# Performance work log

Hardware: AMD Instinct MI355X
Metric: run time of the kernel (lower is better)

The kernel has to match this reference:

```python
import jax, jax.numpy as jnp
import numpy as np

B, H, S, D = 4, 16, 1024, 64
TEMPERATURE = 8.0  # sqrt(D)


def setup_inputs() -> dict:
    key = jax.random.key(0)
    k1, k2, k3, k4, k5, k6 = jax.random.split(key, 6)
    return {
        "q": jax.random.normal(k1, (B, H, S, D), dtype=jnp.float32),
        "k": jax.random.normal(k2, (B, H, S, D), dtype=jnp.float32),
        "v": jax.random.normal(k3, (B, H, S, D), dtype=jnp.float32),
        "mask": jax.random.randint(k4, (B, 1, 1, S), 0, 2, dtype=jnp.int32),
        "adj_matrix": jax.random.normal(k5, (B, S, S), dtype=jnp.float32),
        "dist_matrix": jax.random.uniform(k6, (B, S, S), dtype=jnp.float32),
    }


def reference(q, k, v, mask, adj_matrix, dist_matrix):
    # attn = (q / temperature) @ k^T  -> [B,H,S,S]
    attn = jnp.einsum("bhqd,bhkd->bhqk", q / TEMPERATURE, k)

    # distance-based rescaling: (1 + e) / (1 + exp(1 - dist)), broadcast over heads
    dist = dist_matrix[:, None, :, :]  # [B,1,S,S]
    one = jnp.float32(1.0)
    rescaled = (one + jnp.exp(one)) / (one + jnp.exp(one - dist))
    attn = jax.nn.relu(attn) * rescaled

    # additive adjacency bias, broadcast over heads
    attn = attn + adj_matrix[:, None, :, :]

    # mask fill
    attn = jnp.where(mask == 0, jnp.float32(-1e9), attn)

    attn = jax.nn.softmax(attn, axis=-1)  # dropout p used in eval -> identity
    output = jnp.einsum("bhqk,bhkd->bhqd", attn, v)
    return (output, attn)
```

## Files before the change

kernel.cpp:

```cpp
#include <hip/hip_runtime.h>
#include <hip/hip_bf16.h>

#define NB 4
#define NH 16
#define NS 1024
#define ND 64
#define NBH (NB * NH)
#define NELEM ((size_t)NBH * NS * ND)

typedef __bf16 bf16x8 __attribute__((ext_vector_type(8)));
typedef float f32x4 __attribute__((ext_vector_type(4)));
typedef unsigned short u16x8 __attribute__((ext_vector_type(8)));
typedef unsigned short u16x4 __attribute__((ext_vector_type(4)));


__global__ __launch_bounds__(256) void conv_hilo(const float* __restrict__ src,
                                                 unsigned short* __restrict__ hi,
                                                 unsigned short* __restrict__ lo,
                                                 float scale, int n4) {
    int i = blockIdx.x * 256 + threadIdx.x;
    if (i >= n4) return;
    f32x4 x = ((const f32x4*)src)[i];
    u16x4 h, l;
#pragma unroll
    for (int j = 0; j < 4; ++j) {
        float xs = x[j] * scale;
        __bf16 hb = (__bf16)xs;
        h[j] = __builtin_bit_cast(unsigned short, hb);
        l[j] = __builtin_bit_cast(unsigned short, (__bf16)(xs - (float)hb));
    }
    ((u16x4*)hi)[i] = h;
    ((u16x4*)lo)[i] = l;
}

__global__ __launch_bounds__(256) void conv_vt(const float* __restrict__ V,
                                               unsigned short* __restrict__ Vt) {
    int i = blockIdx.x * 256 + threadIdx.x;
    int bh = i >> 12;
    int kb = (i >> 6) & 63;
    int d  = i & 63;
    const float* vp = V + ((size_t)(bh * NS + kb * 16)) * ND + d;
    unsigned short* op = Vt + ((size_t)(bh * ND + d)) * NS + kb * 16;
    u16x8 o0, o1;
#pragma unroll
    for (int r = 0; r < 8; ++r) o0[r] = __builtin_bit_cast(unsigned short, (__bf16)vp[r * ND]);
#pragma unroll
    for (int r = 0; r < 8; ++r) o1[r] = __builtin_bit_cast(unsigned short, (__bf16)vp[(r + 8) * ND]);
    *(u16x8*)op = o0;
    *(u16x8*)(op + 8) = o1;
}

__global__ __launch_bounds__(256) void fused_attn_pre(
    const unsigned short* __restrict__ Qhi, const unsigned short* __restrict__ Qlo,
    const unsigned short* __restrict__ Khi, const unsigned short* __restrict__ Klo,
    const unsigned short* __restrict__ Vt,
    const int* __restrict__ mask, const float* __restrict__ adj, const float* __restrict__ dist,
    float* __restrict__ out_g, float* __restrict__ attn_g)
{
    const int tid  = (int)threadIdx.x;
    const int lane = tid & 63;
    const int wid  = tid >> 6;
    const int qi   = lane & 15;
    const int g    = lane >> 4;

    int bid = (int)blockIdx.x;
    bid = (bid & 7) * (NBH * 64 / 8) + (bid >> 3);
    const int qt = bid & 63;
    const int bh = bid >> 6;
    const int b  = bh >> 4;

    __shared__ __align__(16) unsigned char smem[4 * 16 * 256 * 2 + 512];
    unsigned short* Plds = (unsigned short*)smem;
    float* red_m = (float*)(smem + 32768);
    float* red_l = red_m + 64;
    typedef float outp_t[16][68];
    outp_t* outp = (outp_t*)smem;

    const int qglob = qt * 16 + qi;
    const int kw    = wid * 256;

    bf16x8 qh[2], ql[2];
    {
        const size_t qo = ((size_t)(bh * NS + qglob)) * ND + g * 8;
        qh[0] = __builtin_bit_cast(bf16x8, *(const u16x8*)(Qhi + qo));
        qh[1] = __builtin_bit_cast(bf16x8, *(const u16x8*)(Qhi + qo + 32));
        ql[0] = __builtin_bit_cast(bf16x8, *(const u16x8*)(Qlo + qo));
        ql[1] = __builtin_bit_cast(bf16x8, *(const u16x8*)(Qlo + qo + 32));
    }

    f32x4 acc[16];
    {
        const f32x4 z = {0.f, 0.f, 0.f, 0.f};
#pragma unroll
        for (int t = 0; t < 16; ++t) acc[t] = z;
    }
#pragma unroll
    for (int t = 0; t < 16; ++t) {
        const size_t ko = ((size_t)(bh * NS + kw + t * 16 + qi)) * ND + g * 8;
#pragma unroll
        for (int c = 0; c < 2; ++c) {
            bf16x8 kh = __builtin_bit_cast(bf16x8, *(const u16x8*)(Khi + ko + c * 32));
            bf16x8 kl = __builtin_bit_cast(bf16x8, *(const u16x8*)(Klo + ko + c * 32));
            acc[t] = __builtin_amdgcn_mfma_f32_16x16x32_bf16(kh, qh[c], acc[t], 0, 0, 0);
            acc[t] = __builtin_amdgcn_mfma_f32_16x16x32_bf16(kl, qh[c], acc[t], 0, 0, 0);
            acc[t] = __builtin_amdgcn_mfma_f32_16x16x32_bf16(kh, ql[c], acc[t], 0, 0, 0);
        }
    }

    const float* adjR  = adj  + ((size_t)(b * NS + qglob)) * NS;
    const float* distR = dist + ((size_t)(b * NS + qglob)) * NS;
    const int*   maskR = mask + b * NS;
    const float  CE = 3.7182817f;

#pragma unroll
    for (int t = 0; t < 16; ++t) {
        const int k0 = kw + t * 16 + g * 4;
        f32x4 a4 = *(const f32x4*)(adjR + k0);
        f32x4 d4 = *(const f32x4*)(distR + k0);
        int4  m4 = *(const int4*)(maskR + k0);
        int   mm[4] = {m4.x, m4.y, m4.z, m4.w};
#pragma unroll
        for (int r = 0; r < 4; ++r) {
            float s = fmaxf(acc[t][r], 0.f);
            float resc = CE * __builtin_amdgcn_rcpf(1.f + __expf(1.f - d4[r]));
            s = s * resc + a4[r];
            acc[t][r] = (mm[r] == 0) ? -1.0e9f : s;
        }
    }

    float m = -3.0e38f;
#pragma unroll
    for (int t = 0; t < 16; ++t)
#pragma unroll
        for (int r = 0; r < 4; ++r) m = fmaxf(m, acc[t][r]);
    m = fmaxf(m, __shfl_xor(m, 16, 64));
    m = fmaxf(m, __shfl_xor(m, 32, 64));
    if (g == 0) red_m[wid * 16 + qi] = m;
    __syncthreads();
    const float mf = fmaxf(fmaxf(red_m[qi], red_m[16 + qi]),
                           fmaxf(red_m[32 + qi], red_m[48 + qi]));

    float l = 0.f;
#pragma unroll
    for (int t = 0; t < 16; ++t)
#pragma unroll
        for (int r = 0; r < 4; ++r) {
            float e = __expf(acc[t][r] - mf);
            acc[t][r] = e;
            l += e;
        }
    l += __shfl_xor(l, 16, 64);
    l += __shfl_xor(l, 32, 64);
    if (g == 0) red_l[wid * 16 + qi] = l;
    __syncthreads();
    const float lf = red_l[qi] + red_l[16 + qi] + red_l[32 + qi] + red_l[48 + qi];
    const float inv = __builtin_amdgcn_rcpf(lf);

    float* attnR = attn_g + ((size_t)(bh * NS + qglob)) * NS;
    unsigned short* Pw = Plds + wid * (16 * 256);
#pragma unroll
    for (int t = 0; t < 16; ++t) {
        const int kloc = t * 16 + g * 4;
        f32x4 e4;
#pragma unroll
        for (int r = 0; r < 4; ++r) e4[r] = acc[t][r] * inv;
        __builtin_nontemporal_store(e4, (f32x4*)(attnR + kw + kloc));

        unsigned int p01 = ((unsigned int)__builtin_bit_cast(unsigned short, (__bf16)e4[0]))
                         | ((unsigned int)__builtin_bit_cast(unsigned short, (__bf16)e4[1]) << 16);
        unsigned int p23 = ((unsigned int)__builtin_bit_cast(unsigned short, (__bf16)e4[2]))
                         | ((unsigned int)__builtin_bit_cast(unsigned short, (__bf16)e4[3]) << 16);
        const int u = kloc >> 2;
        const int c = u >> 1;
        unsigned long long pk = (unsigned long long)p01 | ((unsigned long long)p23 << 32);
        *(unsigned long long*)((char*)Pw + qi * 512 + ((c ^ (qi & 7)) << 4) + (u & 1) * 8) = pk;
    }
    __syncthreads();

    f32x4 o[4];
    {
        const f32x4 z = {0.f, 0.f, 0.f, 0.f};
#pragma unroll
        for (int dt = 0; dt < 4; ++dt) o[dt] = z;
    }
    const unsigned short* vtb = Vt + ((size_t)bh * ND) * NS;
#pragma unroll
    for (int j = 0; j < 8; ++j) {
        const int c = j * 4 + g;
        const u16x8 praw = *(const u16x8*)((const char*)Pw + qi * 512 + ((c ^ (qi & 7)) << 4));
        const bf16x8 pa = __builtin_bit_cast(bf16x8, praw);
#pragma unroll
        for (int dt = 0; dt < 4; ++dt) {
            const bf16x8 vb = __builtin_bit_cast(bf16x8,
                *(const u16x8*)(vtb + (size_t)(dt * 16 + qi) * NS + kw + j * 32 + g * 8));
            o[dt] = __builtin_amdgcn_mfma_f32_16x16x32_bf16(pa, vb, o[dt], 0, 0, 0);
        }
    }
    __syncthreads();

#pragma unroll
    for (int dt = 0; dt < 4; ++dt)
#pragma unroll
        for (int r = 0; r < 4; ++r)
            outp[wid][g * 4 + r][dt * 16 + qi] = o[dt][r];
    __syncthreads();
    {
        const int qrow = tid >> 4;
        const int d0   = (tid & 15) * 4;
        f32x4 s = *(const f32x4*)(&outp[0][qrow][d0]);
#pragma unroll
        for (int w = 1; w < 4; ++w) s += *(const f32x4*)(&outp[w][qrow][d0]);
        __builtin_nontemporal_store(s, (f32x4*)(out_g + ((size_t)(bh * NS + qt * 16 + qrow)) * ND + d0));
    }
}

__global__ __launch_bounds__(256) void fused_attn_kernel(
    const float* __restrict__ Q, const float* __restrict__ K, const float* __restrict__ V,
    const int* __restrict__ mask, const float* __restrict__ adj, const float* __restrict__ dist,
    float* __restrict__ out_g, float* __restrict__ attn_g)
{
    const int tid  = (int)threadIdx.x;
    const int lane = tid & 63;
    const int wid  = tid >> 6;
    const int qi   = lane & 15;
    const int g    = lane >> 4;

    const int bid = (int)blockIdx.x;
    const int qt  = bid & 63;
    const int bh  = bid >> 6;
    const int b   = bh >> 4;

    __shared__ __align__(16) unsigned short Plds[4][16 * 256];
    __shared__ __align__(16) float outp[4][16][68];
    __shared__ float red_m[4][16];
    __shared__ float red_l[4][16];

    const int qglob = qt * 16 + qi;
    const int kw    = wid * 256;

    bf16x8 qh[2], ql[2];
    {
        const float* qp = Q + (bh * NS + qglob) * ND + g * 8;
#pragma unroll
        for (int c = 0; c < 2; ++c) {
            f32x4 f0 = *(const f32x4*)(qp + c * 32);
            f32x4 f1 = *(const f32x4*)(qp + c * 32 + 4);
#pragma unroll
            for (int j = 0; j < 4; ++j) {
                float xh = f0[j] * 0.125f;
                __bf16 hb = (__bf16)xh;
                qh[c][j] = hb; ql[c][j] = (__bf16)(xh - (float)hb);
                float xl = f1[j] * 0.125f;
                __bf16 hb2 = (__bf16)xl;
                qh[c][j + 4] = hb2; ql[c][j + 4] = (__bf16)(xl - (float)hb2);
            }
        }
    }

    f32x4 acc[16];
    {
        const f32x4 z = {0.f, 0.f, 0.f, 0.f};
#pragma unroll
        for (int t = 0; t < 16; ++t) acc[t] = z;
    }
#pragma unroll
    for (int t = 0; t < 16; ++t) {
        const float* kp = K + (bh * NS + kw + t * 16 + qi) * ND + g * 8;
#pragma unroll
        for (int c = 0; c < 2; ++c) {
            f32x4 f0 = *(const f32x4*)(kp + c * 32);
            f32x4 f1 = *(const f32x4*)(kp + c * 32 + 4);
            bf16x8 kh, kl;
#pragma unroll
            for (int j = 0; j < 4; ++j) {
                __bf16 hb = (__bf16)f0[j];
                kh[j] = hb; kl[j] = (__bf16)(f0[j] - (float)hb);
                __bf16 hb2 = (__bf16)f1[j];
                kh[j + 4] = hb2; kl[j + 4] = (__bf16)(f1[j] - (float)hb2);
            }
            acc[t] = __builtin_amdgcn_mfma_f32_16x16x32_bf16(kh, qh[c], acc[t], 0, 0, 0);
            acc[t] = __builtin_amdgcn_mfma_f32_16x16x32_bf16(kl, qh[c], acc[t], 0, 0, 0);
            acc[t] = __builtin_amdgcn_mfma_f32_16x16x32_bf16(kh, ql[c], acc[t], 0, 0, 0);
        }
    }

    const float* adjR  = adj  + (b * NS + qglob) * (size_t)NS;
    const float* distR = dist + (b * NS + qglob) * (size_t)NS;
    const int*   maskR = mask + b * NS;
    const float  CE = 3.7182817f;

#pragma unroll
    for (int t = 0; t < 16; ++t) {
        const int k0 = kw + t * 16 + g * 4;
        f32x4 a4 = *(const f32x4*)(adjR + k0);
        f32x4 d4 = *(const f32x4*)(distR + k0);
        int4  m4 = *(const int4*)(maskR + k0);
        int   mm[4] = {m4.x, m4.y, m4.z, m4.w};
#pragma unroll
        for (int r = 0; r < 4; ++r) {
            float s = fmaxf(acc[t][r], 0.f);
            float resc = CE * __builtin_amdgcn_rcpf(1.f + __expf(1.f - d4[r]));
            s = s * resc + a4[r];
            acc[t][r] = (mm[r] == 0) ? -1.0e9f : s;
        }
    }

    float m = -3.0e38f;
#pragma unroll
    for (int t = 0; t < 16; ++t)
#pragma unroll
        for (int r = 0; r < 4; ++r) m = fmaxf(m, acc[t][r]);
    m = fmaxf(m, __shfl_xor(m, 16, 64));
    m = fmaxf(m, __shfl_xor(m, 32, 64));
    if (g == 0) red_m[wid][qi] = m;
    __syncthreads();
    const float mf = fmaxf(fmaxf(red_m[0][qi], red_m[1][qi]),
                           fmaxf(red_m[2][qi], red_m[3][qi]));

    float l = 0.f;
#pragma unroll
    for (int t = 0; t < 16; ++t)
#pragma unroll
        for (int r = 0; r < 4; ++r) {
            float e = __expf(acc[t][r] - mf);
            acc[t][r] = e;
            l += e;
        }
    l += __shfl_xor(l, 16, 64);
    l += __shfl_xor(l, 32, 64);
    if (g == 0) red_l[wid][qi] = l;
    __syncthreads();
    const float lf = red_l[0][qi] + red_l[1][qi] + red_l[2][qi] + red_l[3][qi];
    const float inv = __builtin_amdgcn_rcpf(lf);

    float* attnR = attn_g + (bh * NS + qglob) * (size_t)NS;
    unsigned short* Pw = &Plds[wid][0];
#pragma unroll
    for (int t = 0; t < 16; ++t) {
        const int kloc = t * 16 + g * 4;
        f32x4 e4;
#pragma unroll
        for (int r = 0; r < 4; ++r) e4[r] = acc[t][r] * inv;
        __builtin_nontemporal_store(e4, (f32x4*)(attnR + kw + kloc));

        unsigned int p01 = ((unsigned int)__builtin_bit_cast(unsigned short, (__bf16)e4[0]))
                         | ((unsigned int)__builtin_bit_cast(unsigned short, (__bf16)e4[1]) << 16);
        unsigned int p23 = ((unsigned int)__builtin_bit_cast(unsigned short, (__bf16)e4[2]))
                         | ((unsigned int)__builtin_bit_cast(unsigned short, (__bf16)e4[3]) << 16);
        const int u = kloc >> 2;
        const int c = u >> 1;
        unsigned long long pk = (unsigned long long)p01 | ((unsigned long long)p23 << 32);
        *(unsigned long long*)((char*)Pw + qi * 512 + ((c ^ (qi & 7)) << 4) + (u & 1) * 8) = pk;
    }
    __syncthreads();

    f32x4 o[4];
    {
        const f32x4 z = {0.f, 0.f, 0.f, 0.f};
#pragma unroll
        for (int dt = 0; dt < 4; ++dt) o[dt] = z;
    }
    const float* vbase = V + (bh * NS + kw) * (size_t)ND;
#pragma unroll
    for (int j = 0; j < 8; ++j) {
        const int c = j * 4 + g;
        const u16x8 praw = *(const u16x8*)((const char*)Pw + qi * 512 + ((c ^ (qi & 7)) << 4));
        const bf16x8 pa = __builtin_bit_cast(bf16x8, praw);
        const float* vp0 = vbase + (j * 32 + g * 8) * ND + qi;
#pragma unroll
        for (int dt = 0; dt < 4; ++dt) {
            bf16x8 vb;
            const float* vp = vp0 + dt * 16;
#pragma unroll
            for (int r = 0; r < 8; ++r) vb[r] = (__bf16)vp[r * ND];
            o[dt] = __builtin_amdgcn_mfma_f32_16x16x32_bf16(pa, vb, o[dt], 0, 0, 0);
        }
    }

#pragma unroll
    for (int dt = 0; dt < 4; ++dt)
#pragma unroll
        for (int r = 0; r < 4; ++r)
            outp[wid][g * 4 + r][dt * 16 + qi] = o[dt][r];
    __syncthreads();
    {
        const int qrow = tid >> 4;
        const int d0   = (tid & 15) * 4;
        f32x4 s = *(const f32x4*)(&outp[0][qrow][d0]);
#pragma unroll
        for (int w = 1; w < 4; ++w) s += *(const f32x4*)(&outp[w][qrow][d0]);
        __builtin_nontemporal_store(s, (f32x4*)(out_g + (bh * NS + qt * 16 + qrow) * (size_t)ND + d0));
    }
}

extern "C" void kernel_launch(void* const* d_in, const int* in_sizes, int n_in,
                              void* d_out, int out_size, void* d_ws, size_t ws_size,
                              hipStream_t stream) {
    const float* Q    = (const float*)d_in[0];
    const float* K    = (const float*)d_in[1];
    const float* V    = (const float*)d_in[2];
    const int*   mask = (const int*)d_in[3];
    const float* adj  = (const float*)d_in[4];
    const float* dist = (const float*)d_in[5];
    float* out  = (float*)d_out;
    float* attn = out + NELEM;

    const size_t need = NELEM * 2 * 5;
    if (ws_size >= need) {
        unsigned short* Qhi = (unsigned short*)d_ws;
        unsigned short* Qlo = Qhi + NELEM;
        unsigned short* Khi = Qlo + NELEM;
        unsigned short* Klo = Khi + NELEM;
        unsigned short* Vt  = Klo + NELEM;
        const int n4 = (int)(NELEM / 4);
        conv_hilo<<<dim3(n4 / 256), 256, 0, stream>>>(Q, Qhi, Qlo, 0.125f, n4);
        conv_hilo<<<dim3(n4 / 256), 256, 0, stream>>>(K, Khi, Klo, 1.0f, n4);
        conv_vt<<<dim3(NBH * ND * (NS / 16) / 256), 256, 0, stream>>>(V, Vt);
        fused_attn_pre<<<dim3(NBH * 64), 256, 0, stream>>>(Qhi, Qlo, Khi, Klo, Vt,
                                                           mask, adj, dist, out, attn);
    } else {
        fused_attn_kernel<<<dim3(NBH * 64), 256, 0, stream>>>(Q, K, V, mask, adj, dist, out, attn);
    }
}
```

Measured before the change: 587.7 us.

## Stage attn writes through LDS for coalesced row stores and interleave QK with epilogue

The attention-probability output is now staged per wave in shared memory with an XOR swizzle, then written back so that each lane stores contiguous 16-byte chunks along a row instead of scattered per-lane row fragments. The QK MFMA chain is folded into the epilogue loop so the K, adj, dist and mask loads for a tile are issued together. Launch bounds now request two blocks per SM. The staging costs extra barriers and LDS traffic, and the occupancy hint may force register spills.

```diff
diff --git a/kernel.cpp b/kernel.cpp
--- a/kernel.cpp
+++ b/kernel.cpp
@@ -50,7 +50,7 @@
     *(u16x8*)(op + 8) = o1;
 }
 
-__global__ __launch_bounds__(256) void fused_attn_pre(
+__global__ __launch_bounds__(256, 2) void fused_attn_pre(
     const unsigned short* __restrict__ Qhi, const unsigned short* __restrict__ Qlo,
     const unsigned short* __restrict__ Khi, const unsigned short* __restrict__ Klo,
     const unsigned short* __restrict__ Vt,
@@ -62,6 +62,8 @@
     const int wid  = tid >> 6;
     const int qi   = lane & 15;
     const int g    = lane >> 4;
+    const int l31  = lane & 31;
+    const int rhalf = lane >> 5;
 
     int bid = (int)blockIdx.x;
     bid = (bid & 7) * (NBH * 64 / 8) + (bid >> 3);
@@ -69,7 +71,7 @@
     const int bh = bid >> 6;
     const int b  = bh >> 4;
 
-    __shared__ __align__(16) unsigned char smem[4 * 16 * 256 * 2 + 512];
+    __shared__ __align__(16) unsigned char smem[4 * 8192 + 512];
     unsigned short* Plds = (unsigned short*)smem;
     float* red_m = (float*)(smem + 32768);
     float* red_l = red_m + 64;
@@ -88,43 +90,40 @@
         ql[1] = __builtin_bit_cast(bf16x8, *(const u16x8*)(Qlo + qo + 32));
     }
 
-    f32x4 acc[16];
-    {
-        const f32x4 z = {0.f, 0.f, 0.f, 0.f};
-#pragma unroll
-        for (int t = 0; t < 16; ++t) acc[t] = z;
-    }
-#pragma unroll
-    for (int t = 0; t < 16; ++t) {
-        const size_t ko = ((size_t)(bh * NS + kw + t * 16 + qi)) * ND + g * 8;
-#pragma unroll
-        for (int c = 0; c < 2; ++c) {
-            bf16x8 kh = __builtin_bit_cast(bf16x8, *(const u16x8*)(Khi + ko + c * 32));
-            bf16x8 kl = __builtin_bit_cast(bf16x8, *(const u16x8*)(Klo + ko + c * 32));
-            acc[t] = __builtin_amdgcn_mfma_f32_16x16x32_bf16(kh, qh[c], acc[t], 0, 0, 0);
-            acc[t] = __builtin_amdgcn_mfma_f32_16x16x32_bf16(kl, qh[c], acc[t], 0, 0, 0);
-            acc[t] = __builtin_amdgcn_mfma_f32_16x16x32_bf16(kh, ql[c], acc[t], 0, 0, 0);
-        }
-    }
-
     const float* adjR  = adj  + ((size_t)(b * NS + qglob)) * NS;
     const float* distR = dist + ((size_t)(b * NS + qglob)) * NS;
     const int*   maskR = mask + b * NS;
     const float  CE = 3.7182817f;
 
+    f32x4 acc[16];
 #pragma unroll
     for (int t = 0; t < 16; ++t) {
+        const size_t ko = ((size_t)(bh * NS + kw + t * 16 + qi)) * ND + g * 8;
+        const bf16x8 kh0 = __builtin_bit_cast(bf16x8, *(const u16x8*)(Khi + ko));
+        const bf16x8 kl0 = __builtin_bit_cast(bf16x8, *(const u16x8*)(Klo + ko));
+        const bf16x8 kh1 = __builtin_bit_cast(bf16x8, *(const u16x8*)(Khi + ko + 32));
+        const bf16x8 kl1 = __builtin_bit_cast(bf16x8, *(const u16x8*)(Klo + ko + 32));
+
         const int k0 = kw + t * 16 + g * 4;
-        f32x4 a4 = *(const f32x4*)(adjR + k0);
-        f32x4 d4 = *(const f32x4*)(distR + k0);
-        int4  m4 = *(const int4*)(maskR + k0);
-        int   mm[4] = {m4.x, m4.y, m4.z, m4.w};
+        const f32x4 a4 = *(const f32x4*)(adjR + k0);
+        const f32x4 d4 = *(const f32x4*)(distR + k0);
+        const int4  m4 = *(const int4*)(maskR + k0);
+
+        f32x4 s = {0.f, 0.f, 0.f, 0.f};
+        s = __builtin_amdgcn_mfma_f32_16x16x32_bf16(kh0, qh[0], s, 0, 0, 0);
+        s = __builtin_amdgcn_mfma_f32_16x16x32_bf16(kl0, qh[0], s, 0, 0, 0);
+        s = __builtin_amdgcn_mfma_f32_16x16x32_bf16(kh0, ql[0], s, 0, 0, 0);
+        s = __builtin_amdgcn_mfma_f32_16x16x32_bf16(kh1, qh[1], s, 0, 0, 0);
+        s = __builtin_amdgcn_mfma_f32_16x16x32_bf16(kl1, qh[1], s, 0, 0, 0);
+        s = __builtin_amdgcn_mfma_f32_16x16x32_bf16(kh1, ql[1], s, 0, 0, 0);
+
+        const int mm[4] = {m4.x, m4.y, m4.z, m4.w};
 #pragma unroll
         for (int r = 0; r < 4; ++r) {
-            float s = fmaxf(acc[t][r], 0.f);
+            float x = fmaxf(s[r], 0.f);
             float resc = CE * __builtin_amdgcn_rcpf(1.f + __expf(1.f - d4[r]));
-            s = s * resc + a4[r];
-            acc[t][r] = (mm[r] == 0) ? -1.0e9f : s;
+            x = x * resc + a4[r];
+            acc[t][r] = (mm[r] == 0) ? -1.0e9f : x;
         }
     }
 
@@ -156,20 +155,39 @@
     const float lf = red_l[qi] + red_l[16 + qi] + red_l[32 + qi] + red_l[48 + qi];
     const float inv = __builtin_amdgcn_rcpf(lf);
 
-    float* attnR = attn_g + ((size_t)(bh * NS + qglob)) * NS;
+    float* stage = (float*)(smem + (size_t)wid * 8192);
+    float* attnRow0 = attn_g + ((size_t)(bh * NS + qt * 16)) * NS + kw;
+#pragma unroll
+    for (int h = 0; h < 2; ++h) {
+        __syncthreads();
+#pragma unroll
+        for (int tl = 0; tl < 8; ++tl) {
+            const int t = h * 8 + tl;
+            f32x4 e4;
+#pragma unroll
+            for (int r = 0; r < 4; ++r) e4[r] = acc[t][r] * inv;
+            const int chunk = (tl * 4 + g) ^ (qi & 7);
+            *(f32x4*)((char*)stage + qi * 512 + chunk * 16) = e4;
+        }
+        __syncthreads();
+#pragma unroll
+        for (int i = 0; i < 8; ++i) {
+            const int r = i * 2 + rhalf;
+            const int chunk = l31 ^ (r & 7);
+            f32x4 v = *(const f32x4*)((const char*)stage + r * 512 + chunk * 16);
+            __builtin_nontemporal_store(v, (f32x4*)(attnRow0 + (size_t)r * NS + h * 128 + l31 * 4));
+        }
+    }
+    __syncthreads();
+
     unsigned short* Pw = Plds + wid * (16 * 256);
 #pragma unroll
     for (int t = 0; t < 16; ++t) {
         const int kloc = t * 16 + g * 4;
-        f32x4 e4;
-#pragma unroll
-        for (int r = 0; r < 4; ++r) e4[r] = acc[t][r] * inv;
-        __builtin_nontemporal_store(e4, (f32x4*)(attnR + kw + kloc));
-
-        unsigned int p01 = ((unsigned int)__builtin_bit_cast(unsigned short, (__bf16)e4[0]))
-                         | ((unsigned int)__builtin_bit_cast(unsigned short, (__bf16)e4[1]) << 16);
-        unsigned int p23 = ((unsigned int)__builtin_bit_cast(unsigned short, (__bf16)e4[2]))
-                         | ((unsigned int)__builtin_bit_cast(unsigned short, (__bf16)e4[3]) << 16);
+        unsigned int p01 = ((unsigned int)__builtin_bit_cast(unsigned short, (__bf16)(acc[t][0] * inv)))
+                         | ((unsigned int)__builtin_bit_cast(unsigned short, (__bf16)(acc[t][1] * inv)) << 16);
+        unsigned int p23 = ((unsigned int)__builtin_bit_cast(unsigned short, (__bf16)(acc[t][2] * inv)))
+                         | ((unsigned int)__builtin_bit_cast(unsigned short, (__bf16)(acc[t][3] * inv)) << 16);
         const int u = kloc >> 2;
         const int c = u >> 1;
         unsigned long long pk = (unsigned long long)p01 | ((unsigned long long)p23 << 32);
@@ -214,7 +232,7 @@
     }
 }
 
-__global__ __launch_bounds__(256) void fused_attn_kernel(
+__global__ __launch_bounds__(256, 2) void fused_attn_kernel(
     const float* __restrict__ Q, const float* __restrict__ K, const float* __restrict__ V,
     const int* __restrict__ mask, const float* __restrict__ adj, const float* __restrict__ dist,
     float* __restrict__ out_g, float* __restrict__ attn_g)
@@ -258,14 +276,10 @@
     }
 
     f32x4 acc[16];
-    {
-        const f32x4 z = {0.f, 0.f, 0.f, 0.f};
-#pragma unroll
-        for (int t = 0; t < 16; ++t) acc[t] = z;
-    }
 #pragma unroll
     for (int t = 0; t < 16; ++t) {
         const float* kp = K + (bh * NS + kw + t * 16 + qi) * ND + g * 8;
+        f32x4 s = {0.f, 0.f, 0.f, 0.f};
 #pragma unroll
         for (int c = 0; c < 2; ++c) {
             f32x4 f0 = *(const f32x4*)(kp + c * 32);
@@ -278,10 +292,11 @@
                 __bf16 hb2 = (__bf16)f1[j];
                 kh[j + 4] = hb2; kl[j + 4] = (__bf16)(f1[j] - (float)hb2);
             }
-            acc[t] = __builtin_amdgcn_mfma_f32_16x16x32_bf16(kh, qh[c], acc[t], 0, 0, 0);
-            acc[t] = __builtin_amdgcn_mfma_f32_16x16x32_bf16(kl, qh[c], acc[t], 0, 0, 0);
-            acc[t] = __builtin_amdgcn_mfma_f32_16x16x32_bf16(kh, ql[c], acc[t], 0, 0, 0);
-        }
+            s = __builtin_amdgcn_mfma_f32_16x16x32_bf16(kh, qh[c], s, 0, 0, 0);
+            s = __builtin_amdgcn_mfma_f32_16x16x32_bf16(kl, qh[c], s, 0, 0, 0);
+            s = __builtin_amdgcn_mfma_f32_16x16x32_bf16(kh, ql[c], s, 0, 0, 0);
+        }
+        acc[t] = s;
     }
 
     const float* adjR  = adj  + (b * NS + qglob) * (size_t)NS;
```

Result: faster. 558.1 us (-5.0%).
